# Optimization experiments

Measured on AMD Instinct MI355X. Metric: run time of the kernel, lower is better.

The kernel has to match this reference:

```python
import jax, jax.numpy as jnp
import numpy as np

EMBED = 1024
HEADS = 16
HEAD_DIM = EMBED // HEADS


def setup_inputs() -> dict:
    key = jax.random.key(0)
    ks = jax.random.split(key, 11)
    B, L, D = 2, 2048, EMBED
    s = 0.02
    return {
        "q": jax.random.normal(ks[0], (B, L, D), jnp.float32),
        "k": jax.random.normal(ks[1], (B, L, D), jnp.float32),
        "v": jax.random.normal(ks[2], (B, L, D), jnp.float32),
        "w_q": jax.random.normal(ks[3], (D, D), jnp.float32) * s,
        "b_q": jnp.zeros((D,), jnp.float32),
        "w_k": jax.random.normal(ks[4], (D, D), jnp.float32) * s,
        "b_k": jnp.zeros((D,), jnp.float32),
        "w_v": jax.random.normal(ks[5], (D, D), jnp.float32) * s,
        "b_v": jnp.zeros((D,), jnp.float32),
        "w_o": jax.random.normal(ks[6], (D, D), jnp.float32) * s,
        "b_o": jnp.zeros((D,), jnp.float32),
    }


def reference(q, k, v, w_q, b_q, w_k, b_k, w_v, b_v, w_o, b_o):
    B, L, D = q.shape
    H, Dh = HEADS, HEAD_DIM
    # Linear projections (torch Linear: x @ W.T + b)
    qp = (q @ w_q.T + b_q).reshape(B, L, H, Dh)
    kp = (k @ w_k.T + b_k).reshape(B, L, H, Dh)
    vp = (v @ w_v.T + b_v).reshape(B, L, H, Dh)
    # energy: [n, h, q, k]
    energy = jnp.einsum("nqhd,nkhd->nhqk", qp, kp)
    scale = 1.0 / jnp.sqrt(jnp.asarray(Dh, qp.dtype))
    attn = jax.nn.softmax(energy * scale, axis=-1)
    ctx = jnp.einsum("nhql,nlhd->nqhd", attn, vp).reshape(B, L, D)
    return ctx @ w_o.T + b_o
```

## Files before the change

kernel.cpp:

```cpp
#include <hip/hip_runtime.h>

typedef __bf16 bf16;
typedef __bf16 bf16x2 __attribute__((ext_vector_type(2)));
typedef __bf16 bf16x4 __attribute__((ext_vector_type(4)));
typedef __bf16 bf16x8 __attribute__((ext_vector_type(8)));
typedef float f32x4 __attribute__((ext_vector_type(4)));

#define MFMA16(a, b, c) __builtin_amdgcn_mfma_f32_16x16x32_bf16((a), (b), (c), 0, 0, 0)

#define QSCALE 0.18033688011112042f

__device__ inline void gld16(const void* g, void* l) {
    __builtin_amdgcn_global_load_lds(
        (const __attribute__((address_space(1))) unsigned int*)g,
        (__attribute__((address_space(3))) unsigned int*)l, 16, 0, 0);
}

__device__ inline bf16x8 cvt8(float4 a, float4 b) {
    bf16x8 v;
    v[0] = (bf16)a.x; v[1] = (bf16)a.y; v[2] = (bf16)a.z; v[3] = (bf16)a.w;
    v[4] = (bf16)b.x; v[5] = (bf16)b.y; v[6] = (bf16)b.z; v[7] = (bf16)b.w;
    return v;
}

__global__ __launch_bounds__(256) void cvt7_kernel(
    const float* __restrict__ q,  bf16* __restrict__ qb,
    const float* __restrict__ k,  bf16* __restrict__ kb,
    const float* __restrict__ v,  bf16* __restrict__ vb,
    const float* __restrict__ wq, bf16* __restrict__ wqb,
    const float* __restrict__ wk, bf16* __restrict__ wkb,
    const float* __restrict__ wv, bf16* __restrict__ wvb,
    const float* __restrict__ wo, bf16* __restrict__ wob)
{
    const float* src; bf16* dst; int n;
    switch (blockIdx.y) {
        case 0: src = q;  dst = qb;  n = 1 << 22; break;
        case 1: src = k;  dst = kb;  n = 1 << 22; break;
        case 2: src = v;  dst = vb;  n = 1 << 22; break;
        case 3: src = wq; dst = wqb; n = 1 << 20; break;
        case 4: src = wk; dst = wkb; n = 1 << 20; break;
        case 5: src = wv; dst = wvb; n = 1 << 20; break;
        default: src = wo; dst = wob; n = 1 << 20; break;
    }
    int i = (blockIdx.x * 256 + threadIdx.x) * 8;
    if (i < n) {
        float4 a = *(const float4*)&src[i];
        float4 b = *(const float4*)&src[i + 4];
        *(bf16x8*)&dst[i] = cvt8(a, b);
    }
}

__global__ __launch_bounds__(256) void cvt3_kernel(
    const float* __restrict__ s0, bf16* __restrict__ d0,
    const float* __restrict__ s1, bf16* __restrict__ d1,
    const float* __restrict__ s2, bf16* __restrict__ d2)
{
    const float* src = blockIdx.y == 0 ? s0 : blockIdx.y == 1 ? s1 : s2;
    bf16*        dst = blockIdx.y == 0 ? d0 : blockIdx.y == 1 ? d1 : d2;
    int i = (blockIdx.x * 256 + threadIdx.x) * 8;
    float4 a = *(const float4*)&src[i];
    float4 b = *(const float4*)&src[i + 4];
    *(bf16x8*)&dst[i] = cvt8(a, b);
}

__global__ __launch_bounds__(256) void cvt_kernel(
    const float* __restrict__ src, bf16* __restrict__ dst, int n)
{
    int i = (blockIdx.x * 256 + threadIdx.x) * 8;
    if (i < n) {
        float4 a = *(const float4*)&src[i];
        float4 b = *(const float4*)&src[i + 4];
        *(bf16x8*)&dst[i] = cvt8(a, b);
    }
}

__global__ __launch_bounds__(256) void qkv_bf16(
    const bf16* __restrict__ qb, const bf16* __restrict__ kb,
    const bf16* __restrict__ vb,
    const bf16* __restrict__ wq, const float* __restrict__ bq,
    const bf16* __restrict__ wk, const float* __restrict__ bk,
    const bf16* __restrict__ wv, const float* __restrict__ bv,
    bf16* __restrict__ Qp, bf16* __restrict__ Kp, bf16* __restrict__ Vt)
{
    __shared__ __align__(16) bf16 sm[16896];
    bf16* As = sm;
    bf16* Bs = sm + 8192;
    bf16* Ts = sm;

    const int id  = blockIdx.x;
    const int pr  = (id >> 6) * 8 + (id & 7);
    const int proj = pr >> 5;
    const int m0  = (pr & 31) * 128;
    const int n0  = ((id >> 3) & 7) * 128;

    const bf16*  A    = proj == 0 ? qb : proj == 1 ? kb : vb;
    const bf16*  B    = proj == 0 ? wq : proj == 1 ? wk : wv;
    const float* bias = proj == 0 ? bq : proj == 1 ? bk : bv;

    const int tid  = threadIdx.x;
    const int lane = tid & 63;
    const int w    = tid >> 6;
    const int g    = lane >> 4;
    const int ln   = lane & 15;
    const int rowb = (w & 1) * 64;
    const int colb = (w >> 1) * 64;
    const int ro   = lane >> 3, lc = lane & 7;

    auto issue = [&](int t) {
        int k0 = t * 64;
        for (int j = 0; j < 4; ++j) {
            int base = w * 32 + j * 8;
            int row  = base + ro;
            int c    = lc ^ (row & 7);
            gld16(&A[(size_t)(m0 + row) * 1024 + k0 + c * 8], &As[base * 64]);
            gld16(&B[(size_t)(n0 + row) * 1024 + k0 + c * 8], &Bs[base * 64]);
        }
    };

    issue(0);
    f32x4 acc[4][4] = {};

    for (int t = 0; t < 16; ++t) {
        __syncthreads();
        for (int ks = 0; ks < 2; ++ks) {
            bf16x8 af[4], bfm[4];
            for (int mi = 0; mi < 4; ++mi) {
                int row = rowb + mi * 16 + ln;
                af[mi] = *(const bf16x8*)&As[row * 64 + ((ks * 4 + g) ^ (ln & 7)) * 8];
            }
            for (int ni = 0; ni < 4; ++ni) {
                int row = colb + ni * 16 + ln;
                bfm[ni] = *(const bf16x8*)&Bs[row * 64 + ((ks * 4 + g) ^ (ln & 7)) * 8];
            }
            for (int mi = 0; mi < 4; ++mi)
                for (int ni = 0; ni < 4; ++ni)
                    acc[mi][ni] = MFMA16(af[mi], bfm[ni], acc[mi][ni]);
        }
        __syncthreads();
        if (t < 15) issue(t + 1);
    }

    if (proj != 2) {
        for (int mi = 0; mi < 4; ++mi) {
            for (int ni = 0; ni < 4; ++ni) {
                int col = n0 + colb + ni * 16 + ln;
                float bv_ = bias[col];
                int rowbase = m0 + rowb + mi * 16 + g * 4;
                if (proj == 0) {
                    for (int r = 0; r < 4; ++r)
                        Qp[(size_t)(rowbase + r) * 1024 + col] =
                            (bf16)((acc[mi][ni][r] + bv_) * QSCALE);
                } else {
                    for (int r = 0; r < 4; ++r)
                        Kp[(size_t)(rowbase + r) * 1024 + col] =
                            (bf16)(acc[mi][ni][r] + bv_);
                }
            }
        }
    } else {
        for (int mi = 0; mi < 4; ++mi) {
            for (int ni = 0; ni < 4; ++ni) {
                int col = colb + ni * 16 + ln;
                float bv_ = bias[n0 + col];
                int row = rowb + mi * 16 + g * 4;
                bf16x4 pk;
                for (int r = 0; r < 4; ++r) pk[r] = (bf16)(acc[mi][ni][r] + bv_);
                *(bf16x4*)&Ts[col * 132 + row] = pk;
            }
        }
        __syncthreads();
        const int bidx = m0 >> 11;
        const int tok0 = m0 & 2047;
        for (int i = 0; i < 8; ++i) {
            int c    = tid + 256 * i;
            int col  = c >> 4;
            int t64  = (c >> 3) & 1;
            int cc   = c & 7;
            int gcol = n0 + col;
            union { bf16 e[8]; uint4 u; } tmp;
            for (int j = 0; j < 8; ++j) {
                int s = 2 * cc + (j >> 2) + ((j & 3) << 4);
                tmp.e[j] = Ts[col * 132 + t64 * 64 + s];
            }
            size_t dst = ((size_t)(bidx * 16 + (gcol >> 6)) * 64 + (gcol & 63)) * 2048
                         + tok0 + t64 * 64 + cc * 8;
            *(uint4*)&Vt[dst] = tmp.u;
        }
    }
}

__global__ __launch_bounds__(256) void qkv_gemm(
    const float* __restrict__ q, const float* __restrict__ k,
    const float* __restrict__ v,
    const bf16* __restrict__ wq, const float* __restrict__ bq,
    const bf16* __restrict__ wk, const float* __restrict__ bk,
    const bf16* __restrict__ wv, const float* __restrict__ bv,
    bf16* __restrict__ Qp, bf16* __restrict__ Kp, bf16* __restrict__ Vt)
{
    __shared__ __align__(16) bf16 sm[8192 + 2 * 8192];
    bf16* As = sm;
    bf16* Bs = sm + 8192;
    bf16* Ts = sm;

    const int id  = blockIdx.x;
    const int pr  = (id >> 6) * 8 + (id & 7);
    const int proj = pr >> 5;
    const int m0  = (pr & 31) * 128;
    const int n0  = ((id >> 3) & 7) * 128;

    const float* A    = proj == 0 ? q  : proj == 1 ? k  : v;
    const bf16*  B    = proj == 0 ? wq : proj == 1 ? wk : wv;
    const float* bias = proj == 0 ? bq : proj == 1 ? bk : bv;

    const int tid  = threadIdx.x;
    const int lane = tid & 63;
    const int w    = tid >> 6;
    const int g    = lane >> 4;
    const int ln   = lane & 15;
    const int rowb = (w & 1) * 64;
    const int colb = (w >> 1) * 64;
    const int srow = tid >> 3, slc = tid & 7;
    const int ro   = lane >> 3, lc = lane & 7;

    float4 ra[4][2];
    for (int i = 0; i < 4; ++i) {
        const float* p = &A[(size_t)(m0 + srow + 32 * i) * 1024 + slc * 8];
        ra[i][0] = *(const float4*)p;
        ra[i][1] = *(const float4*)(p + 4);
    }
    for (int j = 0; j < 4; ++j) {
        int base = w * 32 + j * 8;
        int row  = base + ro;
        int c    = lc ^ (row & 7);
        gld16(&B[(size_t)(n0 + row) * 1024 + c * 8], &Bs[base * 64]);
    }

    f32x4 acc[4][4] = {};

    for (int t = 0; t < 16; ++t) {
        __syncthreads();
        for (int i = 0; i < 4; ++i) {
            int row = srow + 32 * i;
            *(bf16x8*)&As[row * 64 + (slc ^ (row & 7)) * 8] = cvt8(ra[i][0], ra[i][1]);
        }
        __syncthreads();
        if (t < 15) {
            int k1 = (t + 1) * 64;
            for (int i = 0; i < 4; ++i) {
                const float* p = &A[(size_t)(m0 + srow + 32 * i) * 1024 + k1 + slc * 8];
                ra[i][0] = *(const float4*)p;
                ra[i][1] = *(const float4*)(p + 4);
            }
            int bsel = (t + 1) & 1;
            for (int j = 0; j < 4; ++j) {
                int base = w * 32 + j * 8;
                int row  = base + ro;
                int c    = lc ^ (row & 7);
                gld16(&B[(size_t)(n0 + row) * 1024 + k1 + c * 8],
                      &Bs[bsel * 8192 + base * 64]);
            }
        }
        const bf16* Bt = Bs + (t & 1) * 8192;
        for (int ks = 0; ks < 2; ++ks) {
            bf16x8 af[4], bfm[4];
            for (int mi = 0; mi < 4; ++mi) {
                int row = rowb + mi * 16 + ln;
                af[mi] = *(const bf16x8*)&As[row * 64 + ((ks * 4 + g) ^ (ln & 7)) * 8];
            }
            for (int ni = 0; ni < 4; ++ni) {
                int row = colb + ni * 16 + ln;
                bfm[ni] = *(const bf16x8*)&Bt[row * 64 + ((ks * 4 + g) ^ (ln & 7)) * 8];
            }
            for (int mi = 0; mi < 4; ++mi)
                for (int ni = 0; ni < 4; ++ni)
                    acc[mi][ni] = MFMA16(af[mi], bfm[ni], acc[mi][ni]);
        }
    }

    if (proj != 2) {
        for (int mi = 0; mi < 4; ++mi) {
            for (int ni = 0; ni < 4; ++ni) {
                int col = n0 + colb + ni * 16 + ln;
                float bv_ = bias[col];
                int rowbase = m0 + rowb + mi * 16 + g * 4;
                if (proj == 0) {
                    for (int r = 0; r < 4; ++r)
                        Qp[(size_t)(rowbase + r) * 1024 + col] =
                            (bf16)((acc[mi][ni][r] + bv_) * QSCALE);
                } else {
                    for (int r = 0; r < 4; ++r)
                        Kp[(size_t)(rowbase + r) * 1024 + col] =
                            (bf16)(acc[mi][ni][r] + bv_);
                }
            }
        }
    } else {
        __syncthreads();
        for (int mi = 0; mi < 4; ++mi) {
            for (int ni = 0; ni < 4; ++ni) {
                int col = colb + ni * 16 + ln;
                float bv_ = bias[n0 + col];
                int row = rowb + mi * 16 + g * 4;
                bf16x4 pk;
                for (int r = 0; r < 4; ++r) pk[r] = (bf16)(acc[mi][ni][r] + bv_);
                *(bf16x4*)&Ts[col * 132 + row] = pk;
            }
        }
        __syncthreads();
        const int bidx = m0 >> 11;
        const int tok0 = m0 & 2047;
        for (int i = 0; i < 8; ++i) {
            int c    = tid + 256 * i;
            int col  = c >> 4;
            int t64  = (c >> 3) & 1;
            int cc   = c & 7;
            int gcol = n0 + col;
            union { bf16 e[8]; uint4 u; } tmp;
            for (int j = 0; j < 8; ++j) {
                int s = 2 * cc + (j >> 2) + ((j & 3) << 4);
                tmp.e[j] = Ts[col * 132 + t64 * 64 + s];
            }
            size_t dst = ((size_t)(bidx * 16 + (gcol >> 6)) * 64 + (gcol & 63)) * 2048
                         + tok0 + t64 * 64 + cc * 8;
            *(uint4*)&Vt[dst] = tmp.u;
        }
    }
}

__global__ __launch_bounds__(256) void gemm_out(
    const bf16* __restrict__ A, const bf16* __restrict__ B,
    const float* __restrict__ bias, float* __restrict__ C)
{
    __shared__ __align__(16) bf16 sm[2 * 4096 + 2 * 8192];
    bf16* As = sm;
    bf16* Bs = sm + 8192;

    const int id = blockIdx.x;
    const int m0 = ((id >> 6) * 8 + (id & 7)) * 64;
    const int n0 = ((id >> 3) & 7) * 128;

    const int tid  = threadIdx.x;
    const int lane = tid & 63;
    const int w    = tid >> 6;
    const int g    = lane >> 4;
    const int ln   = lane & 15;
    const int rowb = (w & 1) * 32;
    const int colb = (w >> 1) * 64;
    const int ro   = lane >> 3, lc = lane & 7;

    auto issue = [&](int t) {
        int k0 = t * 64, sel = t & 1;
        for (int j = 0; j < 2; ++j) {
            int base = w * 16 + j * 8;
            int row  = base + ro;
            int c    = lc ^ (row & 7);
            gld16(&A[(size_t)(m0 + row) * 1024 + k0 + c * 8],
                  &As[sel * 4096 + base * 64]);
        }
        for (int j = 0; j < 4; ++j) {
            int base = w * 32 + j * 8;
            int row  = base + ro;
            int c    = lc ^ (row & 7);
            gld16(&B[(size_t)(n0 + row) * 1024 + k0 + c * 8],
                  &Bs[sel * 8192 + base * 64]);
        }
    };

    issue(0);
    f32x4 acc[2][4] = {};

    for (int t = 0; t < 16; ++t) {
        __syncthreads();
        if (t < 15) issue(t + 1);
        const bf16* At = As + (t & 1) * 4096;
        const bf16* Bt = Bs + (t & 1) * 8192;
        for (int ks = 0; ks < 2; ++ks) {
            bf16x8 af[2], bfm[4];
            for (int mi = 0; mi < 2; ++mi) {
                int row = rowb + mi * 16 + ln;
                af[mi] = *(const bf16x8*)&At[row * 64 + ((ks * 4 + g) ^ (ln & 7)) * 8];
            }
            for (int ni = 0; ni < 4; ++ni) {
                int row = colb + ni * 16 + ln;
                bfm[ni] = *(const bf16x8*)&Bt[row * 64 + ((ks * 4 + g) ^ (ln & 7)) * 8];
            }
            for (int mi = 0; mi < 2; ++mi)
                for (int ni = 0; ni < 4; ++ni)
                    acc[mi][ni] = MFMA16(af[mi], bfm[ni], acc[mi][ni]);
        }
    }

    for (int mi = 0; mi < 2; ++mi) {
        for (int ni = 0; ni < 4; ++ni) {
            int col = n0 + colb + ni * 16 + ln;
            float bv_ = bias[col];
            int rowbase = m0 + rowb + mi * 16 + g * 4;
            for (int r = 0; r < 4; ++r)
                C[(size_t)(rowbase + r) * 1024 + col] = acc[mi][ni][r] + bv_;
        }
    }
}

__global__ __launch_bounds__(256) void attn_kernel(
    const bf16* __restrict__ Qp, const bf16* __restrict__ Kp,
    const bf16* __restrict__ Vt, bf16* __restrict__ Ctx)
{
    __shared__ __align__(16) bf16 smem[2 * 4096 + 2 * 4096];
    bf16* Ks = smem;
    bf16* Vs = smem + 8192;

    const int id = blockIdx.x;
    const int qt = (id >> 3) & 31;
    const int bh = (id & 7) + ((id >> 8) << 3);

    const int tid  = threadIdx.x;
    const int lane = tid & 63;
    const int w    = tid >> 6;
    const int g    = lane >> 4;
    const int ln   = lane & 15;
    const int ro   = lane >> 3, lc = lane & 7;
    const size_t rowQ0 = (size_t)(bh >> 4) * 2048 + qt * 64;
    const size_t rowK0 = (size_t)(bh >> 4) * 2048;
    const int hcol = (bh & 15) * 64;
    const bf16* VtB = Vt + (size_t)bh * 64 * 2048;

    for (int j = 0; j < 2; ++j) {
        int base = w * 16 + j * 8;
        int row  = base + ro;
        int c    = lc ^ (row & 7);
        gld16(&Kp[(rowK0 + row) * 1024 + hcol + c * 8], &Ks[base * 64]);
        gld16(&VtB[(size_t)row * 2048 + c * 8], &Vs[base * 64]);
    }

    bf16x8 qf[2];
    for (int ks = 0; ks < 2; ++ks)
        qf[ks] = *(const bf16x8*)&Qp[(rowQ0 + w * 16 + ln) * 1024 + hcol
                                     + ks * 32 + g * 8];

    bf16x8 ones;
    for (int i = 0; i < 8; ++i) ones[i] = (bf16)1.0f;

    f32x4 oacc[4] = {};
    f32x4 lacc = {};

    __syncthreads();

    for (int t = 0; t < 32; ++t) {
        if (t < 31) {
            int sel = (t + 1) & 1, kvo = (t + 1) * 64;
            for (int j = 0; j < 2; ++j) {
                int base = w * 16 + j * 8;
                int kv   = base + ro;
                int c    = lc ^ (kv & 7);
                gld16(&Kp[(rowK0 + kvo + kv) * 1024 + hcol + c * 8],
                      &Ks[sel * 4096 + base * 64]);
                gld16(&VtB[(size_t)kv * 2048 + kvo + c * 8],
                      &Vs[sel * 4096 + base * 64]);
            }
        }
        const bf16* Kt  = Ks + (t & 1) * 4096;
        const bf16* Vti = Vs + (t & 1) * 4096;

        f32x4 sf[4] = {};
        for (int ks = 0; ks < 2; ++ks) {
            bf16x8 kf[4];
            for (int nj = 0; nj < 4; ++nj) {
                int row = nj * 16 + ln;
                kf[nj] = *(const bf16x8*)&Kt[row * 64 + ((ks * 4 + g) ^ (ln & 7)) * 8];
            }
            __builtin_amdgcn_s_setprio(1);
            for (int nj = 0; nj < 4; ++nj)
                sf[nj] = MFMA16(kf[nj], qf[ks], sf[nj]);
            __builtin_amdgcn_s_setprio(0);
        }

        unsigned W[4][2];
        for (int r = 0; r < 4; ++r)
            for (int h = 0; h < 2; ++h) {
                bf16x2 t2;
                t2[0] = (bf16)__builtin_amdgcn_exp2f(sf[2 * h][r]);
                t2[1] = (bf16)__builtin_amdgcn_exp2f(sf[2 * h + 1][r]);
                W[r][h] = __builtin_bit_cast(unsigned, t2);
            }
        for (int h = 0; h < 2; ++h) {
            asm("v_permlane16_swap_b32 %0, %1" : "+v"(W[0][h]), "+v"(W[2][h]));
            asm("v_permlane32_swap_b32 %0, %1" : "+v"(W[0][h]), "+v"(W[2][h]));
            asm("v_permlane16_swap_b32 %0, %1" : "+v"(W[1][h]), "+v"(W[3][h]));
            asm("v_permlane32_swap_b32 %0, %1" : "+v"(W[1][h]), "+v"(W[3][h]));
        }

        for (int ks = 0; ks < 2; ++ks) {
            union { unsigned u[4]; bf16x8 v; } pf;
            pf.u[0] = W[2 * ks][0];     pf.u[1] = W[2 * ks][1];
            pf.u[2] = W[2 * ks + 1][0]; pf.u[3] = W[2 * ks + 1][1];
            bf16x8 vf[4];
            for (int nd = 0; nd < 4; ++nd) {
                int row = nd * 16 + ln;
                vf[nd] = *(const bf16x8*)&Vti[row * 64 + ((ks * 4 + g) ^ (ln & 7)) * 8];
            }
            __builtin_amdgcn_s_setprio(1);
            lacc = MFMA16(pf.v, ones, lacc);
            for (int nd = 0; nd < 4; ++nd)
                oacc[nd] = MFMA16(pf.v, vf[nd], oacc[nd]);
            __builtin_amdgcn_s_setprio(0);
        }
        __syncthreads();
    }

    for (int r = 0; r < 4; ++r) {
        float inv = 1.0f / lacc[r];
        size_t row = rowQ0 + w * 16 + g * 4 + r;
        for (int nd = 0; nd < 4; ++nd)
            Ctx[row * 1024 + hcol + nd * 16 + ln] = (bf16)(oacc[nd][r] * inv);
    }
}

extern "C" void kernel_launch(void* const* d_in, const int* in_sizes, int n_in,
                              void* d_out, int out_size, void* d_ws, size_t ws_size,
                              hipStream_t stream)
{
    const float* q  = (const float*)d_in[0];
    const float* k  = (const float*)d_in[1];
    const float* v  = (const float*)d_in[2];
    const float* wq = (const float*)d_in[3];
    const float* bq = (const float*)d_in[4];
    const float* wk = (const float*)d_in[5];
    const float* bk = (const float*)d_in[6];
    const float* wv = (const float*)d_in[7];
    const float* bv = (const float*)d_in[8];
    const float* wo = (const float*)d_in[9];
    const float* bo = (const float*)d_in[10];
    float* out = (float*)d_out;

    const int D = 1024;
    bf16* W  = (bf16*)d_ws;
    bf16* Qp = W;
    bf16* Kp = W + (1u << 22);
    bf16* Vt = W + (2u << 22);
    bf16* Ctx = Qp;

    if (ws_size >= (size_t)40 * 1024 * 1024) {
        bf16* vb  = W + (3u << 22);
        bf16* wqb = W + (1u << 24);
        bf16* wkb = wqb + (1u << 20);
        bf16* wvb = wkb + (1u << 20);
        bf16* wob = wvb + (1u << 20);
        bf16* qb  = (bf16*)d_out;
        bf16* kb  = qb + (1u << 22);

        cvt7_kernel<<<dim3(2048, 7), 256, 0, stream>>>(
            q, qb, k, kb, v, vb, wq, wqb, wk, wkb, wv, wvb, wo, wob);
        qkv_bf16<<<768, 256, 0, stream>>>(qb, kb, vb, wqb, bq, wkb, bk, wvb, bv,
                                          Qp, Kp, Vt);
        attn_kernel<<<1024, 256, 0, stream>>>(Qp, Kp, Vt, Ctx);
        gemm_out<<<512, 256, 0, stream>>>(Ctx, wob, bo, out);
    } else {
        bf16* wqb = (bf16*)d_out;
        bf16* wkb = wqb + (size_t)D * D;
        bf16* wvb = wkb + (size_t)D * D;
        bf16* wob = Kp;

        cvt3_kernel<<<dim3(512, 3), 256, 0, stream>>>(wq, wqb, wk, wkb, wv, wvb);
        qkv_gemm<<<768, 256, 0, stream>>>(q, k, v, wqb, bq, wkb, bk, wvb, bv,
                                          Qp, Kp, Vt);
        attn_kernel<<<1024, 256, 0, stream>>>(Qp, Kp, Vt, Ctx);
        cvt_kernel<<<512, 256, 0, stream>>>(wo, wob, D * D);
        gemm_out<<<512, 256, 0, stream>>>(Ctx, wob, bo, out);
    }
}
```

Before: 221.0 us.

## Process 128 query rows per attention block to reuse each K/V tile twice

Each attention workgroup now handles 128 query rows instead of 64, with every wave holding two 16-row query fragments. Each K and V tile loaded into LDS therefore feeds twice as many MFMAs, halving global K/V traffic and LDS fragment reads per unit of work. The grid halves to 512 blocks and launch bounds request 2 blocks per CU. The cost is more accumulator registers and fewer blocks, which may lower occupancy and latency hiding on a 256-CU part.

Result: faster. 208.4 us (-5.7%).

```diff
diff --git a/kernel.cpp b/kernel.cpp
--- a/kernel.cpp
+++ b/kernel.cpp
@@ -401,7 +401,7 @@
     }
 }
 
-__global__ __launch_bounds__(256) void attn_kernel(
+__global__ __launch_bounds__(256, 2) void attn_kernel(
     const bf16* __restrict__ Qp, const bf16* __restrict__ Kp,
     const bf16* __restrict__ Vt, bf16* __restrict__ Ctx)
 {
@@ -410,8 +410,8 @@
     bf16* Vs = smem + 8192;
 
     const int id = blockIdx.x;
-    const int qt = (id >> 3) & 31;
-    const int bh = (id & 7) + ((id >> 8) << 3);
+    const int qt = (id >> 3) & 15;
+    const int bh = (id & 7) + ((id >> 7) << 3);
 
     const int tid  = threadIdx.x;
     const int lane = tid & 63;
@@ -419,7 +419,7 @@
     const int g    = lane >> 4;
     const int ln   = lane & 15;
     const int ro   = lane >> 3, lc = lane & 7;
-    const size_t rowQ0 = (size_t)(bh >> 4) * 2048 + qt * 64;
+    const size_t rowQ0 = (size_t)(bh >> 4) * 2048 + qt * 128;
     const size_t rowK0 = (size_t)(bh >> 4) * 2048;
     const int hcol = (bh & 15) * 64;
     const bf16* VtB = Vt + (size_t)bh * 64 * 2048;
@@ -432,16 +432,20 @@
         gld16(&VtB[(size_t)row * 2048 + c * 8], &Vs[base * 64]);
     }
 
-    bf16x8 qf[2];
-    for (int ks = 0; ks < 2; ++ks)
-        qf[ks] = *(const bf16x8*)&Qp[(rowQ0 + w * 16 + ln) * 1024 + hcol
-                                     + ks * 32 + g * 8];
+    bf16x8 qf[2][2];
+#pragma unroll
+    for (int u = 0; u < 2; ++u)
+#pragma unroll
+        for (int ks = 0; ks < 2; ++ks)
+            qf[u][ks] = *(const bf16x8*)&Qp[(rowQ0 + w * 32 + u * 16 + ln) * 1024
+                                            + hcol + ks * 32 + g * 8];
 
     bf16x8 ones;
+#pragma unroll
     for (int i = 0; i < 8; ++i) ones[i] = (bf16)1.0f;
 
-    f32x4 oacc[4] = {};
-    f32x4 lacc = {};
+    f32x4 oacc[2][4] = {};
+    f32x4 lacc[2] = {};
 
     __syncthreads();
 
@@ -461,58 +465,80 @@
         const bf16* Kt  = Ks + (t & 1) * 4096;
         const bf16* Vti = Vs + (t & 1) * 4096;
 
-        f32x4 sf[4] = {};
+        f32x4 sf[2][4] = {};
+#pragma unroll
         for (int ks = 0; ks < 2; ++ks) {
             bf16x8 kf[4];
+#pragma unroll
             for (int nj = 0; nj < 4; ++nj) {
                 int row = nj * 16 + ln;
                 kf[nj] = *(const bf16x8*)&Kt[row * 64 + ((ks * 4 + g) ^ (ln & 7)) * 8];
             }
             __builtin_amdgcn_s_setprio(1);
-            for (int nj = 0; nj < 4; ++nj)
-                sf[nj] = MFMA16(kf[nj], qf[ks], sf[nj]);
+#pragma unroll
+            for (int u = 0; u < 2; ++u)
+#pragma unroll
+                for (int nj = 0; nj < 4; ++nj)
+                    sf[u][nj] = MFMA16(kf[nj], qf[u][ks], sf[u][nj]);
             __builtin_amdgcn_s_setprio(0);
         }
 
-        unsigned W[4][2];
-        for (int r = 0; r < 4; ++r)
+        unsigned W[2][4][2];
+#pragma unroll
+        for (int u = 0; u < 2; ++u)
+#pragma unroll
+            for (int r = 0; r < 4; ++r)
+#pragma unroll
+                for (int h = 0; h < 2; ++h) {
+                    bf16x2 t2;
+                    t2[0] = (bf16)__builtin_amdgcn_exp2f(sf[u][2 * h][r]);
+                    t2[1] = (bf16)__builtin_amdgcn_exp2f(sf[u][2 * h + 1][r]);
+                    W[u][r][h] = __builtin_bit_cast(unsigned, t2);
+                }
+#pragma unroll
+        for (int u = 0; u < 2; ++u)
+#pragma unroll
             for (int h = 0; h < 2; ++h) {
-                bf16x2 t2;
-                t2[0] = (bf16)__builtin_amdgcn_exp2f(sf[2 * h][r]);
-                t2[1] = (bf16)__builtin_amdgcn_exp2f(sf[2 * h + 1][r]);
-                W[r][h] = __builtin_bit_cast(unsigned, t2);
-            }
-        for (int h = 0; h < 2; ++h) {
-            asm("v_permlane16_swap_b32 %0, %1" : "+v"(W[0][h]), "+v"(W[2][h]));
-            asm("v_permlane32_swap_b32 %0, %1" : "+v"(W[0][h]), "+v"(W[2][h]));
-            asm("v_permlane16_swap_b32 %0, %1" : "+v"(W[1][h]), "+v"(W[3][h]));
-            asm("v_permlane32_swap_b32 %0, %1" : "+v"(W[1][h]), "+v"(W[3][h]));
-        }
-
+                asm("v_permlane16_swap_b32 %0, %1" : "+v"(W[u][0][h]), "+v"(W[u][2][h]));
+                asm("v_permlane32_swap_b32 %0, %1" : "+v"(W[u][0][h]), "+v"(W[u][2][h]));
+                asm("v_permlane16_swap_b32 %0, %1" : "+v"(W[u][1][h]), "+v"(W[u][3][h]));
+                asm("v_permlane32_swap_b32 %0, %1" : "+v"(W[u][1][h]), "+v"(W[u][3][h]));
+            }
+
+#pragma unroll
         for (int ks = 0; ks < 2; ++ks) {
-            union { unsigned u[4]; bf16x8 v; } pf;
-            pf.u[0] = W[2 * ks][0];     pf.u[1] = W[2 * ks][1];
-            pf.u[2] = W[2 * ks + 1][0]; pf.u[3] = W[2 * ks + 1][1];
             bf16x8 vf[4];
+#pragma unroll
             for (int nd = 0; nd < 4; ++nd) {
                 int row = nd * 16 + ln;
                 vf[nd] = *(const bf16x8*)&Vti[row * 64 + ((ks * 4 + g) ^ (ln & 7)) * 8];
             }
             __builtin_amdgcn_s_setprio(1);
-            lacc = MFMA16(pf.v, ones, lacc);
+#pragma unroll
+            for (int u = 0; u < 2; ++u) {
+                union { unsigned uw[4]; bf16x8 v; } pf;
+                pf.uw[0] = W[u][2 * ks][0];     pf.uw[1] = W[u][2 * ks][1];
+                pf.uw[2] = W[u][2 * ks + 1][0]; pf.uw[3] = W[u][2 * ks + 1][1];
+                lacc[u] = MFMA16(pf.v, ones, lacc[u]);
+#pragma unroll
+                for (int nd = 0; nd < 4; ++nd)
+                    oacc[u][nd] = MFMA16(pf.v, vf[nd], oacc[u][nd]);
+            }
+            __builtin_amdgcn_s_setprio(0);
+        }
+        __syncthreads();
+    }
+
+#pragma unroll
+    for (int u = 0; u < 2; ++u)
+#pragma unroll
+        for (int r = 0; r < 4; ++r) {
+            float inv = 1.0f / lacc[u][r];
+            size_t row = rowQ0 + w * 32 + u * 16 + g * 4 + r;
+#pragma unroll
             for (int nd = 0; nd < 4; ++nd)
-                oacc[nd] = MFMA16(pf.v, vf[nd], oacc[nd]);
-            __builtin_amdgcn_s_setprio(0);
-        }
-        __syncthreads();
-    }
-
-    for (int r = 0; r < 4; ++r) {
-        float inv = 1.0f / lacc[r];
-        size_t row = rowQ0 + w * 16 + g * 4 + r;
-        for (int nd = 0; nd < 4; ++nd)
-            Ctx[row * 1024 + hcol + nd * 16 + ln] = (bf16)(oacc[nd][r] * inv);
-    }
+                Ctx[row * 1024 + hcol + nd * 16 + ln] = (bf16)(oacc[u][nd][r] * inv);
+        }
 }
 
 extern "C" void kernel_launch(void* const* d_in, const int* in_sizes, int n_in,
@@ -552,7 +578,7 @@
             q, qb, k, kb, v, vb, wq, wqb, wk, wkb, wv, wvb, wo, wob);
         qkv_bf16<<<768, 256, 0, stream>>>(qb, kb, vb, wqb, bq, wkb, bk, wvb, bv,
                                           Qp, Kp, Vt);
-        attn_kernel<<<1024, 256, 0, stream>>>(Qp, Kp, Vt, Ctx);
+        attn_kernel<<<512, 256, 0, stream>>>(Qp, Kp, Vt, Ctx);
         gemm_out<<<512, 256, 0, stream>>>(Ctx, wob, bo, out);
     } else {
         bf16* wqb = (bf16*)d_out;
@@ -563,7 +589,7 @@
         cvt3_kernel<<<dim3(512, 3), 256, 0, stream>>>(wq, wqb, wk, wkb, wv, wvb);
         qkv_gemm<<<768, 256, 0, stream>>>(q, k, v, wqb, bq, wkb, bk, wvb, bv,
                                           Qp, Kp, Vt);
-        attn_kernel<<<1024, 256, 0, stream>>>(Qp, Kp, Vt, Ctx);
+        attn_kernel<<<512, 256, 0, stream>>>(Qp, Kp, Vt, Ctx);
         cvt_kernel<<<512, 256, 0, stream>>>(wo, wob, D * D);
         gemm_out<<<512, 256, 0, stream>>>(Ctx, wob, bo, out);
     }
```
